# Performance work log

Hardware: AMD Instinct MI355X
Metric: run time of the kernel (lower is better)

The kernel has to match this reference:

```python
import jax, jax.numpy as jnp
import numpy as np

N, K, D, H = 20000, 32, 256, 8
HD = D // H
DFF = 4 * D
EPS = 1e-5


def _layernorm(x, gamma, beta):
    mu = jnp.mean(x, axis=-1, keepdims=True)
    var = jnp.mean(jnp.square(x - mu), axis=-1, keepdims=True)
    return (x - mu) * jax.lax.rsqrt(var + EPS) * gamma + beta


def setup_inputs() -> dict:
    key = jax.random.key(0)
    ks = jax.random.split(key, 16)
    s = 0.02
    return {
        "x": jax.random.normal(ks[0], (N, D), jnp.float32),
        "attention_samples": jax.random.randint(ks[1], (N, K), 0, N),
        "Wq": jax.random.normal(ks[2], (D, D), jnp.float32) * s,
        "bq": jnp.zeros((D,), jnp.float32),
        "Wk": jax.random.normal(ks[3], (D, D), jnp.float32) * s,
        "bk": jnp.zeros((D,), jnp.float32),
        "Wv": jax.random.normal(ks[4], (D, D), jnp.float32) * s,
        "bv": jnp.zeros((D,), jnp.float32),
        "Wo": jax.random.normal(ks[5], (D, D), jnp.float32) * s,
        "bo": jnp.zeros((D,), jnp.float32),
        "W1": jax.random.normal(ks[6], (D, DFF), jnp.float32) * s,
        "b1": jnp.zeros((DFF,), jnp.float32),
        "W2": jax.random.normal(ks[7], (DFF, D), jnp.float32) * s,
        "b2": jnp.zeros((D,), jnp.float32),
        "g1": jnp.ones((D,), jnp.float32),
        "be1": jnp.zeros((D,), jnp.float32),
        "g2": jnp.ones((D,), jnp.float32),
        "be2": jnp.zeros((D,), jnp.float32),
    }


def reference(x, attention_samples, Wq, bq, Wk, bk, Wv, bv, Wo, bo,
              W1, b1, W2, b2, g1, be1, g2, be2):
    # --- per-node MHA: query = node itself, keys/values = k sampled neighbors ---
    q = (x @ Wq + bq).reshape(N, H, HD)                    # [N,H,hd]
    g = x[attention_samples]                               # [N,K,D] gathered neighbors
    kk = (g @ Wk + bk).reshape(N, K, H, HD)                # [N,K,H,hd]
    vv = (g @ Wv + bv).reshape(N, K, H, HD)
    scale = 1.0 / jnp.sqrt(jnp.asarray(HD, x.dtype))
    scores = jnp.einsum("nhd,nkhd->nhk", q, kk) * scale    # [N,H,K]
    attn = jax.nn.softmax(scores, axis=-1)
    o = jnp.einsum("nhk,nkhd->nhd", attn, vv).reshape(N, D)
    attn_out = o @ Wo + bo                                 # out_proj
    x = _layernorm(x + attn_out, g1, be1)
    # --- FFN ---
    ff = jax.nn.relu(x @ W1 + b1) @ W2 + b2
    x = _layernorm(x + ff, g2, be2)
    return x
```

## Files before the change

kernel.cpp:

```cpp
#include <hip/hip_runtime.h>

#define NN 20000
#define KNEI 32
#define DIM 256
#define NHEAD 8
#define HDIM 32
#define DFFN 1024
#define QKVD 768

typedef __attribute__((ext_vector_type(8))) __bf16 bf16x8;
typedef __attribute__((ext_vector_type(8))) unsigned short u16x8;
typedef __attribute__((ext_vector_type(4))) unsigned short u16x4;
typedef __attribute__((ext_vector_type(4))) float f32x4;
typedef __attribute__((ext_vector_type(2))) float f32x2;

static __device__ __forceinline__ float b2f(unsigned short u) {
    return __builtin_bit_cast(float, (unsigned)u << 16);
}
static __device__ __forceinline__ float blo(unsigned w) {
    return __builtin_bit_cast(float, w << 16);
}
static __device__ __forceinline__ float bhi(unsigned w) {
    return __builtin_bit_cast(float, w & 0xffff0000u);
}
static __device__ __forceinline__ unsigned short f2b(float f) {
    unsigned u = __builtin_bit_cast(unsigned, f);
    return (unsigned short)((u + 0x7fff + ((u >> 16) & 1)) >> 16);
}

static __device__ __forceinline__ unsigned char fp8enc(float v) {
#if defined(__HIP_DEVICE_COMPILE__) && __has_builtin(__builtin_amdgcn_cvt_pk_fp8_f32)
    return (unsigned char)(__builtin_amdgcn_cvt_pk_fp8_f32(v, v, 0u, false) & 0xffu);
#else
    unsigned u = __builtin_bit_cast(unsigned, v);
    unsigned s = u >> 31;
    unsigned a = u & 0x7fffffffu;
    if (a >= 0x43e00000u) return (unsigned char)((s << 7) | 0x7e);
    float af = __builtin_bit_cast(float, a);
    if (af < 0.015625f) {
        unsigned r = (unsigned)(af * 512.0f + 0.5f);
        if (r >= 8u) return (unsigned char)((s << 7) | 0x08);
        return (unsigned char)((s << 7) | r);
    }
    unsigned lsb = (a >> 20) & 1u;
    a += 0x7ffffu + lsb;
    unsigned e = (a >> 23) - 120u;
    unsigned m = (a >> 20) & 7u;
    unsigned code = (e << 3) | m;
    if (code > 0x7eu) code = 0x7eu;
    return (unsigned char)((s << 7) | code);
#endif
}

template<int SEL>
static __device__ __forceinline__ float fp8dec(unsigned word) {
#if defined(__HIP_DEVICE_COMPILE__) && __has_builtin(__builtin_amdgcn_cvt_f32_fp8)
    return __builtin_amdgcn_cvt_f32_fp8(word, SEL);
#else
    unsigned b = (word >> (SEL * 8)) & 0xffu;
    unsigned s = (b >> 7) & 1u;
    unsigned e = (b >> 3) & 0xfu;
    unsigned m = b & 7u;
    float v;
    if (e == 0) v = (float)m * 0.001953125f;
    else        v = __builtin_bit_cast(float, ((e + 120u) << 23) | (m << 20));
    return s ? -v : v;
#endif
}

template<bool HI>
static __device__ __forceinline__ f32x2 fp8pk(unsigned word) {
#if defined(__HIP_DEVICE_COMPILE__) && __has_builtin(__builtin_amdgcn_cvt_pk_f32_fp8)
    return __builtin_amdgcn_cvt_pk_f32_fp8((int)word, HI);
#else
    f32x2 r;
    r.x = fp8dec<HI ? 2 : 0>(word);
    r.y = fp8dec<HI ? 3 : 1>(word);
    return r;
#endif
}

#define GLD16(src, dst)                                                          \
    __builtin_amdgcn_global_load_lds(                                            \
        (const __attribute__((address_space(1))) void*)(const void*)(src),       \
        (__attribute__((address_space(3))) void*)(void*)(dst), 16, 0, 0)

template<int BM, int NT, int RELU, int WF32, int WBF16, int SPLIT>
__global__ __launch_bounds__(256) void gemm_mfma(const unsigned short* __restrict__ A,
                                                 const unsigned short* __restrict__ Bt,
                                                 const float* __restrict__ bias,
                                                 float* __restrict__ Cf,
                                                 unsigned short* __restrict__ Cb,
                                                 unsigned char* __restrict__ kvp,
                                                 int M, int N, int K)
{
    constexpr int BN = 128, BK = 32;
    constexpr int MI = BM / 32;
    constexpr int NI = BN / 32;

    __shared__ unsigned short As[BM * BK];
    __shared__ unsigned short Bs[BN * BK];

    const int tid  = threadIdx.x;
    const int wid  = tid >> 6;
    const int lane = tid & 63;

    const int nwg  = gridDim.x;
    const int orig = blockIdx.x;
    const int xcd  = orig & 7;
    const int pos  = orig >> 3;
    const int qc   = nwg >> 3, rc = nwg & 7;
    const int wgid = (xcd < rc ? xcd * (qc + 1) : rc * (qc + 1) + (xcd - rc) * qc) + pos;
    const int bm = (wgid / NT) * BM;
    const int bn = (wgid % NT) * BN;

    const int wr = (wid >> 1) * (BM / 2);
    const int wc = (wid & 1) * (BN / 2);
    const int r0   = lane & 15;
    const int kblk = (lane >> 4) * 8;

    f32x4 acc[MI][NI];
    #pragma unroll
    for (int i = 0; i < MI; ++i)
        #pragma unroll
        for (int j = 0; j < NI; ++j)
            acc[i][j] = (f32x4){0.f, 0.f, 0.f, 0.f};

    for (int k0 = 0; k0 < K; k0 += BK) {
        #pragma unroll
        for (int t = 0; t < (BM * 4) / 256; ++t) {
            int c = t * 256 + tid;
            int row = bm + (c >> 2);
            if (row >= M) row = M - 1;
            GLD16(A + (size_t)row * K + k0 + (c & 3) * 8,
                  &As[(t * 256 + wid * 64) * 8]);
        }
        #pragma unroll
        for (int t = 0; t < (BN * 4) / 256; ++t) {
            int c = t * 256 + tid;
            GLD16(Bt + (size_t)(bn + (c >> 2)) * K + k0 + (c & 3) * 8,
                  &Bs[(t * 256 + wid * 64) * 8]);
        }
        __syncthreads();

        bf16x8 af[MI], bfr[NI];
        #pragma unroll
        for (int mi = 0; mi < MI; ++mi)
            af[mi] = __builtin_bit_cast(bf16x8,
                     *(const u16x8*)&As[(wr + mi * 16 + r0) * BK + kblk]);
        #pragma unroll
        for (int ni = 0; ni < NI; ++ni)
            bfr[ni] = __builtin_bit_cast(bf16x8,
                     *(const u16x8*)&Bs[(wc + ni * 16 + r0) * BK + kblk]);
        #pragma unroll
        for (int mi = 0; mi < MI; ++mi)
            #pragma unroll
            for (int ni = 0; ni < NI; ++ni)
                acc[mi][ni] = __builtin_amdgcn_mfma_f32_16x16x32_bf16(
                    af[mi], bfr[ni], acc[mi][ni], 0, 0, 0);
        __syncthreads();
    }

    const int r4 = (lane >> 4) * 4;
    #pragma unroll
    for (int mi = 0; mi < MI; ++mi)
        #pragma unroll
        for (int ni = 0; ni < NI; ++ni) {
            const int col = bn + wc + ni * 16 + r0;
            const float bb = bias[col];
            #pragma unroll
            for (int r = 0; r < 4; ++r) {
                const int row = bm + wr + mi * 16 + r4 + r;
                if (row < M) {
                    float v = acc[mi][ni][r] + bb;
                    if (RELU) v = fmaxf(v, 0.f);
                    if (SPLIT) {
                        if (col < 256) {
                            Cb[(size_t)row * DIM + col] = f2b(v);
                        } else {
                            const int cc  = col - 256;
                            const int isV = cc >> 8;
                            const int hh  = (cc & 255) >> 5;
                            const int dd  = cc & 31;
                            kvp[((size_t)(hh >> 1) * NN + row) * 128
                                + isV * 64 + (hh & 1) * 32 + dd] = fp8enc(v);
                        }
                    } else {
                        if (WF32)  Cf[(size_t)row * N + col] = v;
                        if (WBF16) Cb[(size_t)row * N + col] = f2b(v);
                    }
                }
            }
        }
}

template<int RESF32, int WFOUT>
__global__ __launch_bounds__(256) void gemm_ln(const unsigned short* __restrict__ A,
                                               const unsigned short* __restrict__ Bt,
                                               const float* __restrict__ bias,
                                               const float* __restrict__ resf,
                                               const unsigned short* __restrict__ resb,
                                               const float* __restrict__ gamma,
                                               const float* __restrict__ beta,
                                               float* __restrict__ outf,
                                               unsigned short* __restrict__ outb,
                                               int M, int K)
{
    constexpr int BM = 32, BN = 256, BK = 32;
    constexpr int NI = BN / 32;

    __shared__ unsigned short As[BM * BK];
    __shared__ unsigned short Bs[BN * BK];
    __shared__ float rs[2][BM][2];

    const int tid  = threadIdx.x;
    const int wid  = tid >> 6;
    const int lane = tid & 63;
    const int bm = blockIdx.x * BM;
    const int wr = (wid >> 1) * 16;
    const int wc = (wid & 1) * 128;
    const int r0   = lane & 15;
    const int kblk = (lane >> 4) * 8;

    f32x4 acc[NI];
    #pragma unroll
    for (int j = 0; j < NI; ++j) acc[j] = (f32x4){0.f, 0.f, 0.f, 0.f};

    for (int k0 = 0; k0 < K; k0 += BK) {
        if (wid < 2) {
            int c = tid;
            GLD16(A + (size_t)(bm + (c >> 2)) * K + k0 + (c & 3) * 8,
                  &As[(wid * 64) * 8]);
        }
        #pragma unroll
        for (int t = 0; t < 4; ++t) {
            int c = t * 256 + tid;
            GLD16(Bt + (size_t)(c >> 2) * K + k0 + (c & 3) * 8,
                  &Bs[(t * 256 + wid * 64) * 8]);
        }
        __syncthreads();

        bf16x8 af = __builtin_bit_cast(bf16x8,
                    *(const u16x8*)&As[(wr + r0) * BK + kblk]);
        bf16x8 bfr[NI];
        #pragma unroll
        for (int ni = 0; ni < NI; ++ni)
            bfr[ni] = __builtin_bit_cast(bf16x8,
                      *(const u16x8*)&Bs[(wc + ni * 16 + r0) * BK + kblk]);
        #pragma unroll
        for (int ni = 0; ni < NI; ++ni)
            acc[ni] = __builtin_amdgcn_mfma_f32_16x16x32_bf16(af, bfr[ni], acc[ni], 0, 0, 0);
        __syncthreads();
    }

    const int r4 = (lane >> 4) * 4;
    float v[NI][4];
    float rsum[4] = {0.f, 0.f, 0.f, 0.f};
    float rsq[4]  = {0.f, 0.f, 0.f, 0.f};
    #pragma unroll
    for (int ni = 0; ni < NI; ++ni) {
        const int col = wc + ni * 16 + r0;
        const float bb = bias[col];
        #pragma unroll
        for (int r = 0; r < 4; ++r) {
            const size_t idx = (size_t)(bm + wr + r4 + r) * DIM + col;
            const float res = RESF32 ? resf[idx] : b2f(resb[idx]);
            const float val = acc[ni][r] + bb + res;
            v[ni][r] = val;
            rsum[r] += val;
            rsq[r]  += val * val;
        }
    }
    #pragma unroll
    for (int sh = 1; sh <= 8; sh <<= 1) {
        #pragma unroll
        for (int r = 0; r < 4; ++r) {
            rsum[r] += __shfl_xor(rsum[r], sh);
            rsq[r]  += __shfl_xor(rsq[r], sh);
        }
    }
    if (r0 == 0) {
        #pragma unroll
        for (int r = 0; r < 4; ++r) {
            rs[wid & 1][wr + r4 + r][0] = rsum[r];
            rs[wid & 1][wr + r4 + r][1] = rsq[r];
        }
    }
    __syncthreads();
    float mean_r[4], rstd_r[4];
    #pragma unroll
    for (int r = 0; r < 4; ++r) {
        const int lrow = wr + r4 + r;
        const float sum = rs[0][lrow][0] + rs[1][lrow][0];
        const float sq  = rs[0][lrow][1] + rs[1][lrow][1];
        const float mean = sum * (1.f / 256.f);
        mean_r[r] = mean;
        rstd_r[r] = rsqrtf(sq * (1.f / 256.f) - mean * mean + 1e-5f);
    }
    #pragma unroll
    for (int ni = 0; ni < NI; ++ni) {
        const int col = wc + ni * 16 + r0;
        const float g = gamma[col], be = beta[col];
        #pragma unroll
        for (int r = 0; r < 4; ++r) {
            const size_t idx = (size_t)(bm + wr + r4 + r) * DIM + col;
            const float ov = (v[ni][r] - mean_r[r]) * rstd_r[r] * g + be;
            if (WFOUT) outf[idx] = ov;
            else       outb[idx] = f2b(ov);
        }
    }
}

__global__ __launch_bounds__(256) void attn_f8(const unsigned short* __restrict__ q,
                                               const unsigned char* __restrict__ kvp,
                                               const int* __restrict__ samp,
                                               unsigned short* __restrict__ o)
{
    __shared__ int pkbuf[4][128];

    const int bid = blockIdx.x;
    const int hp  = bid & 3;
    const int tid = threadIdx.x;
    const int wid = tid >> 6;
    const int n   = (bid >> 2) * 4 + wid;
    const int lane = tid & 63;
    const int j = lane & 31;
    const int hs = lane >> 5;
    const int h = hp * 2 + hs;

    const int kidx = samp[n * KNEI + j];

    const uint4* qp = (const uint4*)(q + (size_t)n * DIM + h * HDIM);
    const uint4 qa = qp[0], qb = qp[1], qc = qp[2], qd = qp[3];
    const unsigned qw[16] = {qa.x, qa.y, qa.z, qa.w, qb.x, qb.y, qb.z, qb.w,
                             qc.x, qc.y, qc.z, qc.w, qd.x, qd.y, qd.z, qd.w};

    const unsigned char* krow = kvp + ((size_t)hp * NN + kidx) * 128 + hs * 32;
    const uint4 k0 = *(const uint4*)krow;
    const uint4 k1 = *(const uint4*)(krow + 16);
    const unsigned kw[8] = {k0.x, k0.y, k0.z, k0.w, k1.x, k1.y, k1.z, k1.w};

    float s = 0.f;
    #pragma unroll
    for (int i = 0; i < 8; ++i) {
        f32x2 ka = fp8pk<false>(kw[i]);
        f32x2 kb = fp8pk<true>(kw[i]);
        unsigned q0 = qw[2 * i], q1 = qw[2 * i + 1];
        s = fmaf(blo(q0), ka.x, s);
        s = fmaf(bhi(q0), ka.y, s);
        s = fmaf(blo(q1), kb.x, s);
        s = fmaf(bhi(q1), kb.y, s);
    }
    s *= 0.17677669529663687f;

    float m = s;
    #pragma unroll
    for (int sh = 16; sh; sh >>= 1) m = fmaxf(m, __shfl_xor(m, sh));
    float e = __expf(s - m);
    float sum = e;
    #pragma unroll
    for (int sh = 16; sh; sh >>= 1) sum += __shfl_xor(sum, sh);
    const float p = __fdividef(e, sum);

    pkbuf[wid][hs * 64 + j * 2]     = __builtin_bit_cast(int, p);
    pkbuf[wid][hs * 64 + j * 2 + 1] = kidx << 7;

    const int jg = j >> 3, d8 = j & 7;
    const unsigned vconst = (unsigned)((size_t)hp * NN) * 128u + 64u + hs * 32 + d8 * 4;
    float a0 = 0.f, a1 = 0.f, a2 = 0.f, a3 = 0.f;
    #pragma unroll
    for (int jj = 0; jj < 8; ++jj) {
        const int jn = jg * 8 + jj;
        const int2 pk = *(const int2*)&pkbuf[wid][hs * 64 + jn * 2];
        const float pj = __builtin_bit_cast(float, pk.x);
        const unsigned vw = *(const unsigned*)(kvp + vconst + (unsigned)pk.y);
        f32x2 vlo = fp8pk<false>(vw);
        f32x2 vhi = fp8pk<true>(vw);
        a0 = fmaf(pj, vlo.x, a0);
        a1 = fmaf(pj, vlo.y, a1);
        a2 = fmaf(pj, vhi.x, a2);
        a3 = fmaf(pj, vhi.y, a3);
    }
    a0 += __shfl_xor(a0, 8);  a1 += __shfl_xor(a1, 8);
    a2 += __shfl_xor(a2, 8);  a3 += __shfl_xor(a3, 8);
    a0 += __shfl_xor(a0, 16); a1 += __shfl_xor(a1, 16);
    a2 += __shfl_xor(a2, 16); a3 += __shfl_xor(a3, 16);
    if (jg == 0) {
        u16x4 ov = { f2b(a0), f2b(a1), f2b(a2), f2b(a3) };
        *(u16x4*)(o + (size_t)n * DIM + h * HDIM + d8 * 4) = ov;
    }
}

static __device__ __forceinline__ void trans_tile(const float* __restrict__ W,
                                                  unsigned short* __restrict__ T,
                                                  float (*sh)[33],
                                                  int n0, int k0, int N, int K, int tidx)
{
    const int tx = tidx & 31, ty = tidx >> 5;
    #pragma unroll
    for (int i = 0; i < 32; i += 8)
        sh[ty + i][tx] = W[(size_t)(k0 + ty + i) * N + n0 + tx];
    __syncthreads();
    #pragma unroll
    for (int i = 0; i < 32; i += 8)
        T[(size_t)(n0 + ty + i) * K + k0 + tx] = f2b(sh[tx][ty + i]);
}

__global__ __launch_bounds__(256) void prep_all(const float* __restrict__ Wq,
                                                const float* __restrict__ Wk,
                                                const float* __restrict__ Wv,
                                                const float* __restrict__ Wo,
                                                const float* __restrict__ W1,
                                                const float* __restrict__ W2,
                                                const float* __restrict__ bq,
                                                const float* __restrict__ bk,
                                                const float* __restrict__ bv,
                                                const float* __restrict__ x,
                                                unsigned short* __restrict__ WqkvT,
                                                unsigned short* __restrict__ WoT,
                                                unsigned short* __restrict__ W1T,
                                                unsigned short* __restrict__ W2T,
                                                float* __restrict__ bqkv,
                                                unsigned short* __restrict__ xb)
{
    __shared__ float sh[32][33];
    const int bid = blockIdx.x;
    const int tidx = threadIdx.x;

    if (bid < 256) {
        const float* W; unsigned short* T;
        switch (bid >> 6) {
            case 0:  W = Wq; T = WqkvT;           break;
            case 1:  W = Wk; T = WqkvT + 65536;   break;
            case 2:  W = Wv; T = WqkvT + 131072;  break;
            default: W = Wo; T = WoT;             break;
        }
        const int t = bid & 63;
        trans_tile(W, T, sh, (t & 7) * 32, (t >> 3) * 32, DIM, DIM, tidx);
    } else if (bid < 512) {
        const int t = bid - 256;
        trans_tile(W1, W1T, sh, (t & 31) * 32, (t >> 5) * 32, DFFN, DIM, tidx);
    } else if (bid < 768) {
        const int t = bid - 512;
        trans_tile(W2, W2T, sh, (t & 7) * 32, (t >> 3) * 32, DIM, DFFN, tidx);
    } else if (bid == 768) {
        if (tidx < 256) {
            bqkv[tidx]       = bq[tidx];
            bqkv[tidx + 256] = bk[tidx];
            bqkv[tidx + 512] = bv[tidx];
        }
    } else {
        const int i = (bid - 769) * 256 + tidx;
        if (i < NN * DIM / 4) {
            float4 v = ((const float4*)x)[i];
            u16x4 b = { f2b(v.x), f2b(v.y), f2b(v.z), f2b(v.w) };
            ((u16x4*)xb)[i] = b;
        }
    }
}

extern "C" void kernel_launch(void* const* d_in, const int* in_sizes, int n_in,
                              void* d_out, int out_size, void* d_ws, size_t ws_size,
                              hipStream_t stream)
{
    const float* x    = (const float*)d_in[0];
    const int*   samp = (const int*)  d_in[1];
    const float* Wq = (const float*)d_in[2];  const float* bq = (const float*)d_in[3];
    const float* Wk = (const float*)d_in[4];  const float* bk = (const float*)d_in[5];
    const float* Wv = (const float*)d_in[6];  const float* bv = (const float*)d_in[7];
    const float* Wo = (const float*)d_in[8];  const float* bo = (const float*)d_in[9];
    const float* W1 = (const float*)d_in[10]; const float* b1 = (const float*)d_in[11];
    const float* W2 = (const float*)d_in[12]; const float* b2 = (const float*)d_in[13];
    const float* g1 = (const float*)d_in[14]; const float* be1 = (const float*)d_in[15];
    const float* g2 = (const float*)d_in[16]; const float* be2 = (const float*)d_in[17];
    float* out = (float*)d_out;

    char* w = (char*)d_ws;
    const size_t MB = 1u << 20;
    unsigned short* WqkvT = (unsigned short*)(w + 0);
    unsigned short* WoT   = (unsigned short*)(w + 393216);
    unsigned short* W1T   = (unsigned short*)(w + 524288);
    unsigned short* W2T   = (unsigned short*)(w + 1048576);
    float*          bqkv  = (float*)(w + 1572864);
    unsigned short* xb    = (unsigned short*)(w + 2 * MB);
    unsigned short* qb    = (unsigned short*)(w + 13 * MB);
    unsigned char*  kvp   = (unsigned char*) (w + 24 * MB);
    unsigned short* ob    = xb;
    unsigned short* x1b   = (unsigned short*)(w + 46 * MB);
    unsigned short* hmid  = (unsigned short*)(w + 57 * MB);

    const dim3 blk(256);

    prep_all<<<dim3(769 + NN * DIM / 4 / 256), blk, 0, stream>>>(
        Wq, Wk, Wv, Wo, W1, W2, bq, bk, bv, x,
        WqkvT, WoT, W1T, W2T, bqkv, xb);

    gemm_mfma<128, 6, 0, 0, 0, 1><<<dim3(157 * 6), blk, 0, stream>>>(
        xb, WqkvT, bqkv, nullptr, qb, kvp, NN, QKVD, DIM);

    attn_f8<<<dim3(NN), blk, 0, stream>>>(qb, kvp, samp, ob);

    gemm_ln<1, 0><<<dim3(NN / 32), blk, 0, stream>>>(
        ob, WoT, bo, x, nullptr, g1, be1, nullptr, x1b, NN, DIM);

    gemm_mfma<128, 8, 1, 0, 1, 0><<<dim3(157 * 8), blk, 0, stream>>>(
        x1b, W1T, b1, nullptr, hmid, nullptr, NN, DFFN, DIM);

    gemm_ln<0, 1><<<dim3(NN / 32), blk, 0, stream>>>(
        hmid, W2T, b2, nullptr, x1b, g2, be2, out, nullptr, NN, DFFN);
}
```

Before: 157.3 us.

## Process two nodes per wave in attention and use bf16 residual in out-proj

The attention kernel now handles two nodes per wavefront, batching the K and Q loads and the V gathers for both so more memory requests are in flight, and launches half as many blocks. The attention output gets its own buffer instead of overwriting xb. This lets the out-projection LayerNorm kernel read the residual from bf16 xb rather than fp32 x, halving that read traffic at some cost in residual precision. The per-thread register use in the attention kernel roughly doubles, which may lower occupancy.

After: 159.3 us. Within noise of the previous version (+1.3%).

```diff
diff --git a/kernel.cpp b/kernel.cpp
--- a/kernel.cpp
+++ b/kernel.cpp
@@ -316,78 +316,100 @@
                                                const int* __restrict__ samp,
                                                unsigned short* __restrict__ o)
 {
-    __shared__ int pkbuf[4][128];
+    __shared__ int pkbuf[4][2][128];
 
     const int bid = blockIdx.x;
     const int hp  = bid & 3;
     const int tid = threadIdx.x;
     const int wid = tid >> 6;
-    const int n   = (bid >> 2) * 4 + wid;
     const int lane = tid & 63;
     const int j = lane & 31;
     const int hs = lane >> 5;
     const int h = hp * 2 + hs;
-
-    const int kidx = samp[n * KNEI + j];
-
-    const uint4* qp = (const uint4*)(q + (size_t)n * DIM + h * HDIM);
-    const uint4 qa = qp[0], qb = qp[1], qc = qp[2], qd = qp[3];
-    const unsigned qw[16] = {qa.x, qa.y, qa.z, qa.w, qb.x, qb.y, qb.z, qb.w,
-                             qc.x, qc.y, qc.z, qc.w, qd.x, qd.y, qd.z, qd.w};
-
-    const unsigned char* krow = kvp + ((size_t)hp * NN + kidx) * 128 + hs * 32;
-    const uint4 k0 = *(const uint4*)krow;
-    const uint4 k1 = *(const uint4*)(krow + 16);
-    const unsigned kw[8] = {k0.x, k0.y, k0.z, k0.w, k1.x, k1.y, k1.z, k1.w};
-
-    float s = 0.f;
-    #pragma unroll
-    for (int i = 0; i < 8; ++i) {
-        f32x2 ka = fp8pk<false>(kw[i]);
-        f32x2 kb = fp8pk<true>(kw[i]);
-        unsigned q0 = qw[2 * i], q1 = qw[2 * i + 1];
-        s = fmaf(blo(q0), ka.x, s);
-        s = fmaf(bhi(q0), ka.y, s);
-        s = fmaf(blo(q1), kb.x, s);
-        s = fmaf(bhi(q1), kb.y, s);
-    }
-    s *= 0.17677669529663687f;
-
-    float m = s;
-    #pragma unroll
-    for (int sh = 16; sh; sh >>= 1) m = fmaxf(m, __shfl_xor(m, sh));
-    float e = __expf(s - m);
-    float sum = e;
-    #pragma unroll
-    for (int sh = 16; sh; sh >>= 1) sum += __shfl_xor(sum, sh);
-    const float p = __fdividef(e, sum);
-
-    pkbuf[wid][hs * 64 + j * 2]     = __builtin_bit_cast(int, p);
-    pkbuf[wid][hs * 64 + j * 2 + 1] = kidx << 7;
+    const int nbase = (bid >> 2) * 8 + wid * 2;
+
+    int kidx[2];
+    #pragma unroll
+    for (int u = 0; u < 2; ++u) kidx[u] = samp[(nbase + u) * KNEI + j];
+
+    uint4 k0[2], k1[2];
+    #pragma unroll
+    for (int u = 0; u < 2; ++u) {
+        const unsigned char* krow = kvp + ((size_t)hp * NN + kidx[u]) * 128 + hs * 32;
+        k0[u] = *(const uint4*)krow;
+        k1[u] = *(const uint4*)(krow + 16);
+    }
+    uint4 qv[2][4];
+    #pragma unroll
+    for (int u = 0; u < 2; ++u) {
+        const uint4* qp = (const uint4*)(q + (size_t)(nbase + u) * DIM + h * HDIM);
+        qv[u][0] = qp[0]; qv[u][1] = qp[1]; qv[u][2] = qp[2]; qv[u][3] = qp[3];
+    }
+
+    #pragma unroll
+    for (int u = 0; u < 2; ++u) {
+        const unsigned qw[16] = {qv[u][0].x, qv[u][0].y, qv[u][0].z, qv[u][0].w,
+                                 qv[u][1].x, qv[u][1].y, qv[u][1].z, qv[u][1].w,
+                                 qv[u][2].x, qv[u][2].y, qv[u][2].z, qv[u][2].w,
+                                 qv[u][3].x, qv[u][3].y, qv[u][3].z, qv[u][3].w};
+        const unsigned kw[8] = {k0[u].x, k0[u].y, k0[u].z, k0[u].w,
+                                k1[u].x, k1[u].y, k1[u].z, k1[u].w};
+        float s = 0.f;
+        #pragma unroll
+        for (int i = 0; i < 8; ++i) {
+            f32x2 ka = fp8pk<false>(kw[i]);
+            f32x2 kb = fp8pk<true>(kw[i]);
+            unsigned q0 = qw[2 * i], q1 = qw[2 * i + 1];
+            s = fmaf(blo(q0), ka.x, s);
+            s = fmaf(bhi(q0), ka.y, s);
+            s = fmaf(blo(q1), kb.x, s);
+            s = fmaf(bhi(q1), kb.y, s);
+        }
+        s *= 0.17677669529663687f;
+
+        float m = s;
+        #pragma unroll
+        for (int sh = 16; sh; sh >>= 1) m = fmaxf(m, __shfl_xor(m, sh));
+        float e = __expf(s - m);
+        float sum = e;
+        #pragma unroll
+        for (int sh = 16; sh; sh >>= 1) sum += __shfl_xor(sum, sh);
+        const float p = __fdividef(e, sum);
+
+        pkbuf[wid][u][hs * 64 + j * 2]     = __builtin_bit_cast(int, p);
+        pkbuf[wid][u][hs * 64 + j * 2 + 1] = kidx[u] << 7;
+    }
 
     const int jg = j >> 3, d8 = j & 7;
     const unsigned vconst = (unsigned)((size_t)hp * NN) * 128u + 64u + hs * 32 + d8 * 4;
-    float a0 = 0.f, a1 = 0.f, a2 = 0.f, a3 = 0.f;
+    float a[2][4] = {};
     #pragma unroll
     for (int jj = 0; jj < 8; ++jj) {
-        const int jn = jg * 8 + jj;
-        const int2 pk = *(const int2*)&pkbuf[wid][hs * 64 + jn * 2];
-        const float pj = __builtin_bit_cast(float, pk.x);
-        const unsigned vw = *(const unsigned*)(kvp + vconst + (unsigned)pk.y);
-        f32x2 vlo = fp8pk<false>(vw);
-        f32x2 vhi = fp8pk<true>(vw);
-        a0 = fmaf(pj, vlo.x, a0);
-        a1 = fmaf(pj, vlo.y, a1);
-        a2 = fmaf(pj, vhi.x, a2);
-        a3 = fmaf(pj, vhi.y, a3);
-    }
-    a0 += __shfl_xor(a0, 8);  a1 += __shfl_xor(a1, 8);
-    a2 += __shfl_xor(a2, 8);  a3 += __shfl_xor(a3, 8);
-    a0 += __shfl_xor(a0, 16); a1 += __shfl_xor(a1, 16);
-    a2 += __shfl_xor(a2, 16); a3 += __shfl_xor(a3, 16);
-    if (jg == 0) {
-        u16x4 ov = { f2b(a0), f2b(a1), f2b(a2), f2b(a3) };
-        *(u16x4*)(o + (size_t)n * DIM + h * HDIM + d8 * 4) = ov;
+        #pragma unroll
+        for (int u = 0; u < 2; ++u) {
+            const int jn = jg * 8 + jj;
+            const int2 pk = *(const int2*)&pkbuf[wid][u][hs * 64 + jn * 2];
+            const float pj = __builtin_bit_cast(float, pk.x);
+            const unsigned vw = *(const unsigned*)(kvp + vconst + (unsigned)pk.y);
+            f32x2 vlo = fp8pk<false>(vw);
+            f32x2 vhi = fp8pk<true>(vw);
+            a[u][0] = fmaf(pj, vlo.x, a[u][0]);
+            a[u][1] = fmaf(pj, vlo.y, a[u][1]);
+            a[u][2] = fmaf(pj, vhi.x, a[u][2]);
+            a[u][3] = fmaf(pj, vhi.y, a[u][3]);
+        }
+    }
+    #pragma unroll
+    for (int u = 0; u < 2; ++u) {
+        #pragma unroll
+        for (int r = 0; r < 4; ++r) {
+            a[u][r] += __shfl_xor(a[u][r], 8);
+            a[u][r] += __shfl_xor(a[u][r], 16);
+        }
+        if (jg == 0) {
+            u16x4 ov = { f2b(a[u][0]), f2b(a[u][1]), f2b(a[u][2]), f2b(a[u][3]) };
+            *(u16x4*)(o + (size_t)(nbase + u) * DIM + h * HDIM + d8 * 4) = ov;
+        }
     }
 }
 
@@ -485,7 +507,7 @@
     unsigned short* xb    = (unsigned short*)(w + 2 * MB);
     unsigned short* qb    = (unsigned short*)(w + 13 * MB);
     unsigned char*  kvp   = (unsigned char*) (w + 24 * MB);
-    unsigned short* ob    = xb;
+    unsigned short* ob    = (unsigned short*)(w + 35 * MB);
     unsigned short* x1b   = (unsigned short*)(w + 46 * MB);
     unsigned short* hmid  = (unsigned short*)(w + 57 * MB);
 
@@ -498,10 +520,10 @@
     gemm_mfma<128, 6, 0, 0, 0, 1><<<dim3(157 * 6), blk, 0, stream>>>(
         xb, WqkvT, bqkv, nullptr, qb, kvp, NN, QKVD, DIM);
 
-    attn_f8<<<dim3(NN), blk, 0, stream>>>(qb, kvp, samp, ob);
-
-    gemm_ln<1, 0><<<dim3(NN / 32), blk, 0, stream>>>(
-        ob, WoT, bo, x, nullptr, g1, be1, nullptr, x1b, NN, DIM);
+    attn_f8<<<dim3(NN / 2), blk, 0, stream>>>(qb, kvp, samp, ob);
+
+    gemm_ln<0, 0><<<dim3(NN / 32), blk, 0, stream>>>(
+        ob, WoT, bo, nullptr, xb, g1, be1, nullptr, x1b, NN, DIM);
 
     gemm_mfma<128, 8, 1, 0, 1, 0><<<dim3(157 * 8), blk, 0, stream>>>(
         x1b, W1T, b1, nullptr, hmid, nullptr, NN, DFFN, DIM);
```
